# Kernel optimization log

Measured on AMD Instinct MI355X. Metric: run time of the kernel, lower is better.

## Reference

```python
import jax, jax.numpy as jnp
import numpy as np

EPS = 0.05
THRESH = 1e-6
MAX_ITER = 100


def _l2norm(x):
    # matches torch F.normalize(dim=-1): x / max(||x||, 1e-12)
    n = jnp.sqrt(jnp.sum(x * x, axis=-1, keepdims=True))
    return x / jnp.maximum(n, 1e-12)


def setup_inputs() -> dict:
    key = jax.random.key(0)
    kq, kk, kv = jax.random.split(key, 3)
    B, N, D = 8, 1024, 64
    return {
        "q": jax.random.normal(kq, (B, N, D), dtype=jnp.float32),
        "k": jax.random.normal(kk, (B, N, D), dtype=jnp.float32),
        "V": jax.random.normal(kv, (B, N, D), dtype=jnp.float32),
    }


def reference(q, k, V):
    B, N, D = q.shape
    Q = _l2norm(q)
    Kn = _l2norm(k)
    # cost matrix: 1 - cosine similarity, shape (B, N, N)
    C = 1.0 - jnp.einsum("bnd,bmd->bnm", Q, Kn)

    log_mu = jnp.full((B, N), jnp.log(1.0 / N + 1e-8), dtype=C.dtype)
    log_nu = log_mu

    def kernel(u, v):
        # (-C + u_i + v_j) / eps, shape (B, N, N)
        return (-C + u[:, :, None] + v[:, None, :]) / EPS

    def step(carry, _):
        u, v, done = carry
        u0 = u
        u_new = EPS * (log_mu - jax.scipy.special.logsumexp(kernel(u, v), axis=2)) + u
        v_new = EPS * (log_nu - jax.scipy.special.logsumexp(kernel(u_new, v), axis=1)) + v
        err = jnp.mean(jnp.abs(u_new - u0))
        # replicate torch early-break: once converged, freeze u, v
        u = jnp.where(done, u, u_new)
        v = jnp.where(done, v, v_new)
        done = jnp.logical_or(done, err < THRESH)
        return (u, v, done), None

    u0 = jnp.zeros((B, N), dtype=C.dtype)
    v0 = jnp.zeros((B, N), dtype=C.dtype)
    (u, v, _), _ = jax.lax.scan(
        jax.checkpoint(step), (u0, v0, jnp.array(False)), None, length=MAX_ITER
    )

    T = jnp.exp(kernel(u, v))  # transport plan (B, N, N)
    out = jnp.einsum("bnm,bmd->bnd", T, V) + V
    return out
```

## Files before the change

kernel.cpp:

```cpp
#include <hip/hip_runtime.h>
#include <math.h>

#define BB 8
#define NN 1024
#define DD 64
#define EPSF 0.05f
#define MAX_ITER 100
#define ERR_SUM_THRESH 8.192e-3f
#define SCALE_ 28.853900817779268f
#define EPSLN2_ 0.034657359027997264f
#define NBLK 256
#define NPER 32

typedef __attribute__((ext_vector_type(8))) short short8;
typedef __attribute__((ext_vector_type(4))) float f32x4;

static __device__ __forceinline__ float fexp2(float x) { return __builtin_amdgcn_exp2f(x); }
static __device__ __forceinline__ float flog2(float x) { return __builtin_amdgcn_logf(x); }
static __device__ __forceinline__ float bflo(unsigned u) { return __uint_as_float(u << 16); }
static __device__ __forceinline__ unsigned short bf16rne(float x) {
    unsigned u = __float_as_uint(x);
    u += 0x7fffu + ((u >> 16) & 1u);
    return (unsigned short)(u >> 16);
}
__device__ __forceinline__ float wave_sum64(float x) {
#pragma unroll
    for (int off = 1; off < 64; off <<= 1) x += __shfl_xor(x, off);
    return x;
}

#define ERRIDX(t, b) ((b) * 128 + (t))
#define CNTIDX(p, b) ((b) * 256 + (p))
#define PUBIDX(t) (t)

__global__ __launch_bounds__(256) void cost_kernel(const float* __restrict__ q,
                                                   const float* __restrict__ k,
                                                   unsigned short* __restrict__ M,
                                                   unsigned short* __restrict__ MT) {
    __shared__ __align__(16) float Qs[64][65];
    __shared__ __align__(16) float Ks[64][65];
    __shared__ float qin[64];
    __shared__ float kin[64];
    __shared__ __align__(16) unsigned short Qb[64][72];
    __shared__ __align__(16) unsigned short Kb[64][72];
    int b = blockIdx.z;
    int i0 = blockIdx.y * 64, j0 = blockIdx.x * 64;
    const float* Qp = q + ((size_t)b * NN + i0) * DD;
    const float* Kp = k + ((size_t)b * NN + j0) * DD;
    int tid = threadIdx.x;
#pragma unroll
    for (int kk = 0; kk < 4; ++kk) {
        int c = tid + 256 * kk;
        int row = c >> 4;
        int c4 = c & 15;
        float4 qv = ((const float4*)(Qp + row * DD))[c4];
        Qs[row][c4 * 4 + 0] = qv.x; Qs[row][c4 * 4 + 1] = qv.y;
        Qs[row][c4 * 4 + 2] = qv.z; Qs[row][c4 * 4 + 3] = qv.w;
        float4 kv = ((const float4*)(Kp + row * DD))[c4];
        Ks[row][c4 * 4 + 0] = kv.x; Ks[row][c4 * 4 + 1] = kv.y;
        Ks[row][c4 * 4 + 2] = kv.z; Ks[row][c4 * 4 + 3] = kv.w;
    }
    __syncthreads();
    if (tid < 64) {
        float ss = 0.f;
#pragma unroll 16
        for (int d = 0; d < 64; ++d) ss += Qs[tid][d] * Qs[tid][d];
        qin[tid] = 1.0f / fmaxf(sqrtf(ss), 1e-12f);
    } else if (tid < 128) {
        int r = tid - 64;
        float ss = 0.f;
#pragma unroll 16
        for (int d = 0; d < 64; ++d) ss += Ks[r][d] * Ks[r][d];
        kin[r] = 1.0f / fmaxf(sqrtf(ss), 1e-12f);
    }
    __syncthreads();
    {
        int row = tid >> 2, d0 = (tid & 3) * 16;
        float qs = qin[row], ks = kin[row];
#pragma unroll
        for (int p = 0; p < 4; ++p) {
            int d = d0 + p * 4;
            uint2 t;
            t.x = (unsigned)bf16rne(Qs[row][d + 0] * qs) | ((unsigned)bf16rne(Qs[row][d + 1] * qs) << 16);
            t.y = (unsigned)bf16rne(Qs[row][d + 2] * qs) | ((unsigned)bf16rne(Qs[row][d + 3] * qs) << 16);
            *(uint2*)&Qb[row][d] = t;
            t.x = (unsigned)bf16rne(Ks[row][d + 0] * ks) | ((unsigned)bf16rne(Ks[row][d + 1] * ks) << 16);
            t.y = (unsigned)bf16rne(Ks[row][d + 2] * ks) | ((unsigned)bf16rne(Ks[row][d + 3] * ks) << 16);
            *(uint2*)&Kb[row][d] = t;
        }
    }
    __syncthreads();
    int w = tid >> 6, lane = tid & 63;
    int m = lane & 15, qq = lane >> 4;
    int rloc = w * 16;
    short8 a0 = *(const short8*)&Qb[rloc + m][qq * 8];
    short8 a1 = *(const short8*)&Qb[rloc + m][qq * 8 + 32];
    f32x4 acc[4];
#pragma unroll
    for (int nt = 0; nt < 4; ++nt) {
        short8 b0 = *(const short8*)&Kb[nt * 16 + m][qq * 8];
        short8 b1 = *(const short8*)&Kb[nt * 16 + m][qq * 8 + 32];
        f32x4 z = {0.f, 0.f, 0.f, 0.f};
        z = __builtin_amdgcn_mfma_f32_16x16x32_bf16(a0, b0, z, 0, 0, 0);
        acc[nt] = __builtin_amdgcn_mfma_f32_16x16x32_bf16(a1, b1, z, 0, 0, 0);
    }
#pragma unroll
    for (int nt = 0; nt < 4; ++nt) {
        int gj = j0 + nt * 16 + m;
        unsigned short us[4];
#pragma unroll
        for (int r = 0; r < 4; ++r)
            us[r] = bf16rne(fexp2((acc[nt][r] - 1.0f) * SCALE_));
#pragma unroll
        for (int r = 0; r < 4; ++r)
            M[((size_t)b << 20) + ((size_t)(i0 + rloc + qq * 4 + r) << 10) + gj] = us[r];
        uint2 t;
        t.x = (unsigned)us[0] | ((unsigned)us[1] << 16);
        t.y = (unsigned)us[2] | ((unsigned)us[3] << 16);
        *(uint2*)(MT + ((size_t)b << 20) + ((size_t)gj << 10) + i0 + rloc + qq * 4) = t;
    }
}

#define ACC8(U4, base)                                              \
    s0 = fmaf(bflo(U4.x), wrg[base + 0], s0);                       \
    s1 = fmaf(__uint_as_float(U4.x), wrg[base + 1], s1);            \
    s0 = fmaf(bflo(U4.y), wrg[base + 2], s0);                       \
    s1 = fmaf(__uint_as_float(U4.y), wrg[base + 3], s1);            \
    s0 = fmaf(bflo(U4.z), wrg[base + 4], s0);                       \
    s1 = fmaf(__uint_as_float(U4.z), wrg[base + 5], s1);            \
    s0 = fmaf(bflo(U4.w), wrg[base + 6], s0);                       \
    s1 = fmaf(__uint_as_float(U4.w), wrg[base + 7], s1);

__global__ __launch_bounds__(256, 1) void sink_coop(const unsigned short* __restrict__ M,
                                                    const unsigned short* __restrict__ MT,
                                                    float* __restrict__ u,
                                                    float* __restrict__ v,
                                                    float* __restrict__ err,
                                                    unsigned* __restrict__ cnt,
                                                    unsigned* __restrict__ pub,
                                                    float eln) {
    __shared__ __align__(16) float sw[1280];
    __shared__ float sdel[4];
    __shared__ int sflag;
    int tid = threadIdx.x;
    int w = tid >> 6, lane = tid & 63;
    int b = blockIdx.x & 7;
    int slice = blockIdx.x >> 3;
    int rbase = slice * 32 + w * 8;
    const unsigned short* Mb  = M  + ((size_t)b << 20);
    const unsigned short* MTb = MT + ((size_t)b << 20);
    float* ub = u + (b << 10);
    float* vb = v + (b << 10);

    uint4 mA[8], mB[8], nA[8], nB[8];
#pragma unroll
    for (int r = 0; r < 8; ++r) {
        const uint4* rp = (const uint4*)(Mb + ((size_t)(rbase + r) << 10));
        mA[r] = rp[lane * 2];
        mB[r] = rp[lane * 2 + 1];
        const uint4* tp = (const uint4*)(MTb + ((size_t)(rbase + r) << 10));
        nA[r] = tp[lane * 2];
        nB[r] = tp[lane * 2 + 1];
    }

    float uprev[8];
#pragma unroll
    for (int r = 0; r < 8; ++r) uprev[r] = 0.f;

    for (int t = 0; t < MAX_ITER; ++t) {
        {
            float4 ex;
            ex.x = fexp2(__hip_atomic_load(vb + tid * 4 + 0, __ATOMIC_RELAXED, __HIP_MEMORY_SCOPE_AGENT) * SCALE_);
            ex.y = fexp2(__hip_atomic_load(vb + tid * 4 + 1, __ATOMIC_RELAXED, __HIP_MEMORY_SCOPE_AGENT) * SCALE_);
            ex.z = fexp2(__hip_atomic_load(vb + tid * 4 + 2, __ATOMIC_RELAXED, __HIP_MEMORY_SCOPE_AGENT) * SCALE_);
            ex.w = fexp2(__hip_atomic_load(vb + tid * 4 + 3, __ATOMIC_RELAXED, __HIP_MEMORY_SCOPE_AGENT) * SCALE_);
            *(float4*)&sw[tid * 4 + 4 * (tid >> 2)] = ex;
            __syncthreads();
            float wrg[16];
            *(float4*)&wrg[0]  = *(const float4*)&sw[lane * 20 + 0];
            *(float4*)&wrg[4]  = *(const float4*)&sw[lane * 20 + 4];
            *(float4*)&wrg[8]  = *(const float4*)&sw[lane * 20 + 8];
            *(float4*)&wrg[12] = *(const float4*)&sw[lane * 20 + 12];
            float del = 0.f;
#pragma unroll
            for (int rr = 0; rr < 8; ++rr) {
                float s0 = 0.f, s1 = 0.f;
                ACC8(mA[rr], 0)
                ACC8(mB[rr], 8)
                float s = wave_sum64(s0 + s1);
                float un = eln - EPSLN2_ * flog2(s);
                del += fabsf(un - uprev[rr]);
                uprev[rr] = un;
                if (lane == 0)
                    __hip_atomic_store(ub + rbase + rr, un, __ATOMIC_RELAXED, __HIP_MEMORY_SCOPE_AGENT);
            }
            if (lane == 0) sdel[w] = del;
            asm volatile("s_waitcnt vmcnt(0)" ::: "memory");
            __syncthreads();
            if (tid == 0) {
                __hip_atomic_fetch_add(err + ERRIDX(t, b), sdel[0] + sdel[1] + sdel[2] + sdel[3],
                                       __ATOMIC_RELAXED, __HIP_MEMORY_SCOPE_AGENT);
                asm volatile("s_waitcnt vmcnt(0)" ::: "memory");
                unsigned* c = cnt + CNTIDX(2 * t, b);
                __hip_atomic_fetch_add(c, 1u, __ATOMIC_RELAXED, __HIP_MEMORY_SCOPE_AGENT);
                while (__hip_atomic_load(c, __ATOMIC_RELAXED, __HIP_MEMORY_SCOPE_AGENT) < NPER)
                    __builtin_amdgcn_s_sleep(1);
                if (slice == 0) {
                    asm volatile("s_waitcnt vmcnt(0)" ::: "memory");
                    __hip_atomic_fetch_add(pub + PUBIDX(t), 1u, __ATOMIC_RELAXED, __HIP_MEMORY_SCOPE_AGENT);
                }
            }
            __syncthreads();
        }
        {
            float4 ex;
            ex.x = fexp2(__hip_atomic_load(ub + tid * 4 + 0, __ATOMIC_RELAXED, __HIP_MEMORY_SCOPE_AGENT) * SCALE_);
            ex.y = fexp2(__hip_atomic_load(ub + tid * 4 + 1, __ATOMIC_RELAXED, __HIP_MEMORY_SCOPE_AGENT) * SCALE_);
            ex.z = fexp2(__hip_atomic_load(ub + tid * 4 + 2, __ATOMIC_RELAXED, __HIP_MEMORY_SCOPE_AGENT) * SCALE_);
            ex.w = fexp2(__hip_atomic_load(ub + tid * 4 + 3, __ATOMIC_RELAXED, __HIP_MEMORY_SCOPE_AGENT) * SCALE_);
            *(float4*)&sw[tid * 4 + 4 * (tid >> 2)] = ex;
            __syncthreads();
            float wrg[16];
            *(float4*)&wrg[0]  = *(const float4*)&sw[lane * 20 + 0];
            *(float4*)&wrg[4]  = *(const float4*)&sw[lane * 20 + 4];
            *(float4*)&wrg[8]  = *(const float4*)&sw[lane * 20 + 8];
            *(float4*)&wrg[12] = *(const float4*)&sw[lane * 20 + 12];
#pragma unroll
            for (int rr = 0; rr < 8; ++rr) {
                float s0 = 0.f, s1 = 0.f;
                ACC8(nA[rr], 0)
                ACC8(nB[rr], 8)
                float s = wave_sum64(s0 + s1);
                float vn = eln - EPSLN2_ * flog2(s);
                if (lane == 0)
                    __hip_atomic_store(vb + rbase + rr, vn, __ATOMIC_RELAXED, __HIP_MEMORY_SCOPE_AGENT);
            }
            asm volatile("s_waitcnt vmcnt(0)" ::: "memory");
            __syncthreads();
            if (tid == 0) {
                unsigned* c = cnt + CNTIDX(2 * t + 1, b);
                __hip_atomic_fetch_add(c, 1u, __ATOMIC_RELAXED, __HIP_MEMORY_SCOPE_AGENT);
                while (__hip_atomic_load(c, __ATOMIC_RELAXED, __HIP_MEMORY_SCOPE_AGENT) < NPER)
                    __builtin_amdgcn_s_sleep(1);
                float eb = __hip_atomic_load(err + ERRIDX(t, b), __ATOMIC_RELAXED, __HIP_MEMORY_SCOPE_AGENT);
                int brk = 0;
                if (eb < ERR_SUM_THRESH) {
                    while (__hip_atomic_load(pub + PUBIDX(t), __ATOMIC_RELAXED, __HIP_MEMORY_SCOPE_AGENT) < 8u)
                        __builtin_amdgcn_s_sleep(1);
                    float s = 0.f;
                    for (int bb = 0; bb < 8; ++bb)
                        s += __hip_atomic_load(err + ERRIDX(t, bb), __ATOMIC_RELAXED, __HIP_MEMORY_SCOPE_AGENT);
                    brk = (s < ERR_SUM_THRESH);
                }
                sflag = brk;
            }
            __syncthreads();
            if (sflag) break;
        }
    }
}

__global__ __launch_bounds__(256) void wt_kernel(const float* __restrict__ V,
                                                 const float* __restrict__ v,
                                                 unsigned short* __restrict__ WT) {
    __shared__ __align__(16) float Vs[64][65];
    __shared__ float wj[64];
    int b = blockIdx.x & 7, jt = blockIdx.x >> 3;
    int j0 = jt * 64;
    int tid = threadIdx.x;
    const float* Vb = V + ((size_t)b << 16) + ((size_t)j0 << 6);
#pragma unroll
    for (int c = 0; c < 4; ++c) {
        int idx = tid + 256 * c;
        int row = idx >> 4, c4 = idx & 15;
        float4 x = ((const float4*)(Vb + row * 64))[c4];
        Vs[row][c4 * 4 + 0] = x.x; Vs[row][c4 * 4 + 1] = x.y;
        Vs[row][c4 * 4 + 2] = x.z; Vs[row][c4 * 4 + 3] = x.w;
    }
    if (tid < 64) wj[tid] = fexp2(v[(b << 10) + j0 + tid] * SCALE_);
    __syncthreads();
    int d = tid >> 2, qd = tid & 3;
    unsigned pk[8];
#pragma unroll
    for (int p = 0; p < 8; ++p) {
        int j = qd * 16 + p * 2;
        unsigned lo = bf16rne(Vs[j][d] * wj[j]);
        unsigned hi = bf16rne(Vs[j + 1][d] * wj[j + 1]);
        pk[p] = lo | (hi << 16);
    }
    unsigned short* dst = WT + ((size_t)b << 16) + ((size_t)d << 10) + j0 + qd * 16;
    ((uint4*)dst)[0] = make_uint4(pk[0], pk[1], pk[2], pk[3]);
    ((uint4*)dst)[1] = make_uint4(pk[4], pk[5], pk[6], pk[7]);
}

__global__ __launch_bounds__(256) void gemm_final(const unsigned short* __restrict__ M,
                                                  const unsigned short* __restrict__ WT,
                                                  const float* __restrict__ u,
                                                  const float* __restrict__ V,
                                                  float* __restrict__ out) {
    __shared__ float sa[32];
    int tid = threadIdx.x;
    int w = tid >> 6, lane = tid & 63;
    int b = blockIdx.x & 7, mt = blockIdx.x >> 3;
    if (tid < 32) sa[tid] = fexp2(u[(b << 10) + mt * 32 + tid] * SCALE_);
    __syncthreads();
    int m = lane & 15, q = lane >> 4;
    int rloc = (w & 1) * 16;
    int nbase = (w >> 1) * 32;
    const unsigned short* Ma = M + ((size_t)b << 20) + ((size_t)(mt * 32 + rloc + m) << 10) + q * 8;
    const unsigned short* W0 = WT + ((size_t)b << 16) + ((size_t)(nbase + m) << 10) + q * 8;
    const unsigned short* W1 = W0 + (16 << 10);
    f32x4 acc0 = {0.f, 0.f, 0.f, 0.f}, acc1 = {0.f, 0.f, 0.f, 0.f};
#pragma unroll 4
    for (int k0 = 0; k0 < NN; k0 += 32) {
        short8 af = *(const short8*)(Ma + k0);
        short8 b0 = *(const short8*)(W0 + k0);
        short8 b1 = *(const short8*)(W1 + k0);
        acc0 = __builtin_amdgcn_mfma_f32_16x16x32_bf16(af, b0, acc0, 0, 0, 0);
        acc1 = __builtin_amdgcn_mfma_f32_16x16x32_bf16(af, b1, acc1, 0, 0, 0);
    }
#pragma unroll
    for (int r = 0; r < 4; ++r) {
        int lrow = rloc + q * 4 + r;
        int gm = mt * 32 + lrow;
        float a = sa[lrow];
        size_t base = (((size_t)b << 10) + gm) * DD;
        int n0 = nbase + m;
        out[base + n0]      = fmaf(a, acc0[r], V[base + n0]);
        out[base + n0 + 16] = fmaf(a, acc1[r], V[base + n0 + 16]);
    }
}

extern "C" void kernel_launch(void* const* d_in, const int* in_sizes, int n_in,
                              void* d_out, int out_size, void* d_ws, size_t ws_size,
                              hipStream_t stream) {
    const float* q = (const float*)d_in[0];
    const float* k = (const float*)d_in[1];
    const float* V = (const float*)d_in[2];
    float* out = (float*)d_out;

    char* ws = (char*)d_ws;
    const size_t MB16 = (size_t)BB * NN * NN * sizeof(unsigned short);
    unsigned short* M  = (unsigned short*)ws;
    unsigned short* MT = (unsigned short*)(ws + MB16);
    unsigned short* WT = MT;
    float* u   = (float*)(ws + 2 * MB16);
    float* v   = u + BB * NN;
    float* err = v + BB * NN;
    unsigned* cnt = (unsigned*)(err + 1024);
    unsigned* pub = cnt + 2048;

    size_t zbytes = (size_t)(2 * BB * NN + 1024 + 2048 + 128) * 4;
    hipMemsetAsync(u, 0, zbytes, stream);

    cost_kernel<<<dim3(16, 16, 8), 256, 0, stream>>>(q, k, M, MT);

    float eln = EPSF * logf(1.0f / NN + 1e-8f);
    sink_coop<<<dim3(NBLK), dim3(256), 0, stream>>>(M, MT, u, v, err, cnt, pub, eln);

    wt_kernel<<<128, 256, 0, stream>>>(V, v, WT);
    gemm_final<<<256, 256, 0, stream>>>(M, WT, u, V, out);
}
```

Baseline: 189.9 us.

## Fuse final transport-plan GEMM into persistent Sinkhorn kernel, drop wt and gemm kernels

Removes the separate wt_kernel and MFMA gemm_final launches. After the Sinkhorn loop exits, each cooperative block loads the final v, scales its own rows of M by exp(v), and multiplies by V with scalar FMAs staged through LDS, adding the V residual. This saves two kernel launches and the WT round trip through global memory. In exchange, the MFMA GEMM becomes a CUDA-core FP32 loop over 1024x64 per row group, and there is no grid-wide barrier before v is read, which risks reading stale v from other blocks.

```diff
diff --git a/kernel.cpp b/kernel.cpp
--- a/kernel.cpp
+++ b/kernel.cpp
@@ -18,6 +18,7 @@
 static __device__ __forceinline__ float fexp2(float x) { return __builtin_amdgcn_exp2f(x); }
 static __device__ __forceinline__ float flog2(float x) { return __builtin_amdgcn_logf(x); }
 static __device__ __forceinline__ float bflo(unsigned u) { return __uint_as_float(u << 16); }
+static __device__ __forceinline__ float bfu(unsigned short s) { return __uint_as_float(((unsigned)s) << 16); }
 static __device__ __forceinline__ unsigned short bf16rne(float x) {
     unsigned u = __float_as_uint(x);
     u += 0x7fffu + ((u >> 16) & 1u);
@@ -32,6 +33,7 @@
 #define ERRIDX(t, b) ((b) * 128 + (t))
 #define CNTIDX(p, b) ((b) * 256 + (p))
 #define PUBIDX(t) (t)
+#define SWIDX2(j) ((j) + 4 * ((j) >> 4))
 
 __global__ __launch_bounds__(256) void cost_kernel(const float* __restrict__ q,
                                                    const float* __restrict__ k,
@@ -138,10 +140,13 @@
                                                     float* __restrict__ err,
                                                     unsigned* __restrict__ cnt,
                                                     unsigned* __restrict__ pub,
+                                                    const float* __restrict__ V,
+                                                    float* __restrict__ out,
                                                     float eln) {
     __shared__ __align__(16) float sw[1280];
     __shared__ float sdel[4];
     __shared__ int sflag;
+    __shared__ __align__(16) float sP[4][64][8];
     int tid = threadIdx.x;
     int w = tid >> 6, lane = tid & 63;
     int b = blockIdx.x & 7;
@@ -258,76 +263,54 @@
             if (sflag) break;
         }
     }
-}
-
-__global__ __launch_bounds__(256) void wt_kernel(const float* __restrict__ V,
-                                                 const float* __restrict__ v,
-                                                 unsigned short* __restrict__ WT) {
-    __shared__ __align__(16) float Vs[64][65];
-    __shared__ float wj[64];
-    int b = blockIdx.x & 7, jt = blockIdx.x >> 3;
-    int j0 = jt * 64;
-    int tid = threadIdx.x;
-    const float* Vb = V + ((size_t)b << 16) + ((size_t)j0 << 6);
-#pragma unroll
-    for (int c = 0; c < 4; ++c) {
-        int idx = tid + 256 * c;
-        int row = idx >> 4, c4 = idx & 15;
-        float4 x = ((const float4*)(Vb + row * 64))[c4];
-        Vs[row][c4 * 4 + 0] = x.x; Vs[row][c4 * 4 + 1] = x.y;
-        Vs[row][c4 * 4 + 2] = x.z; Vs[row][c4 * 4 + 3] = x.w;
-    }
-    if (tid < 64) wj[tid] = fexp2(v[(b << 10) + j0 + tid] * SCALE_);
-    __syncthreads();
-    int d = tid >> 2, qd = tid & 3;
-    unsigned pk[8];
-#pragma unroll
-    for (int p = 0; p < 8; ++p) {
-        int j = qd * 16 + p * 2;
-        unsigned lo = bf16rne(Vs[j][d] * wj[j]);
-        unsigned hi = bf16rne(Vs[j + 1][d] * wj[j + 1]);
-        pk[p] = lo | (hi << 16);
-    }
-    unsigned short* dst = WT + ((size_t)b << 16) + ((size_t)d << 10) + j0 + qd * 16;
-    ((uint4*)dst)[0] = make_uint4(pk[0], pk[1], pk[2], pk[3]);
-    ((uint4*)dst)[1] = make_uint4(pk[4], pk[5], pk[6], pk[7]);
-}
-
-__global__ __launch_bounds__(256) void gemm_final(const unsigned short* __restrict__ M,
-                                                  const unsigned short* __restrict__ WT,
-                                                  const float* __restrict__ u,
-                                                  const float* __restrict__ V,
-                                                  float* __restrict__ out) {
-    __shared__ float sa[32];
-    int tid = threadIdx.x;
-    int w = tid >> 6, lane = tid & 63;
-    int b = blockIdx.x & 7, mt = blockIdx.x >> 3;
-    if (tid < 32) sa[tid] = fexp2(u[(b << 10) + mt * 32 + tid] * SCALE_);
-    __syncthreads();
-    int m = lane & 15, q = lane >> 4;
-    int rloc = (w & 1) * 16;
-    int nbase = (w >> 1) * 32;
-    const unsigned short* Ma = M + ((size_t)b << 20) + ((size_t)(mt * 32 + rloc + m) << 10) + q * 8;
-    const unsigned short* W0 = WT + ((size_t)b << 16) + ((size_t)(nbase + m) << 10) + q * 8;
-    const unsigned short* W1 = W0 + (16 << 10);
-    f32x4 acc0 = {0.f, 0.f, 0.f, 0.f}, acc1 = {0.f, 0.f, 0.f, 0.f};
-#pragma unroll 4
-    for (int k0 = 0; k0 < NN; k0 += 32) {
-        short8 af = *(const short8*)(Ma + k0);
-        short8 b0 = *(const short8*)(W0 + k0);
-        short8 b1 = *(const short8*)(W1 + k0);
-        acc0 = __builtin_amdgcn_mfma_f32_16x16x32_bf16(af, b0, acc0, 0, 0, 0);
-        acc1 = __builtin_amdgcn_mfma_f32_16x16x32_bf16(af, b1, acc1, 0, 0, 0);
-    }
-#pragma unroll
-    for (int r = 0; r < 4; ++r) {
-        int lrow = rloc + q * 4 + r;
-        int gm = mt * 32 + lrow;
-        float a = sa[lrow];
-        size_t base = (((size_t)b << 10) + gm) * DD;
-        int n0 = nbase + m;
-        out[base + n0]      = fmaf(a, acc0[r], V[base + n0]);
-        out[base + n0 + 16] = fmaf(a, acc1[r], V[base + n0 + 16]);
+
+    __syncthreads();
+    {
+        float4 ex;
+        ex.x = fexp2(__hip_atomic_load(vb + tid * 4 + 0, __ATOMIC_RELAXED, __HIP_MEMORY_SCOPE_AGENT) * SCALE_);
+        ex.y = fexp2(__hip_atomic_load(vb + tid * 4 + 1, __ATOMIC_RELAXED, __HIP_MEMORY_SCOPE_AGENT) * SCALE_);
+        ex.z = fexp2(__hip_atomic_load(vb + tid * 4 + 2, __ATOMIC_RELAXED, __HIP_MEMORY_SCOPE_AGENT) * SCALE_);
+        ex.w = fexp2(__hip_atomic_load(vb + tid * 4 + 3, __ATOMIC_RELAXED, __HIP_MEMORY_SCOPE_AGENT) * SCALE_);
+        *(float4*)&sw[tid * 4 + 4 * (tid >> 2)] = ex;
+    }
+    __syncthreads();
+    const float* Vb = V + ((size_t)b << 16);
+    float a8[8];
+#pragma unroll
+    for (int r = 0; r < 8; ++r) a8[r] = fexp2(uprev[r] * SCALE_);
+    float acc[8] = {0.f, 0.f, 0.f, 0.f, 0.f, 0.f, 0.f, 0.f};
+    for (int j0 = 0; j0 < NN; j0 += 64) {
+        float vt[64];
+#pragma unroll
+        for (int jj = 0; jj < 64; ++jj) vt[jj] = Vb[(size_t)(j0 + jj) * DD + lane];
+        float wl = sw[SWIDX2(j0 + lane)];
+        float p[8];
+#pragma unroll
+        for (int r = 0; r < 8; ++r)
+            p[r] = bfu(Mb[((size_t)(rbase + r) << 10) + j0 + lane]) * wl;
+        asm volatile("s_waitcnt lgkmcnt(0)" ::: "memory");
+        *(float4*)&sP[w][lane][0] = make_float4(p[0], p[1], p[2], p[3]);
+        *(float4*)&sP[w][lane][4] = make_float4(p[4], p[5], p[6], p[7]);
+        asm volatile("s_waitcnt lgkmcnt(0)" ::: "memory");
+#pragma unroll
+        for (int jj = 0; jj < 64; ++jj) {
+            float4 pA = *(const float4*)&sP[w][jj][0];
+            float4 pB = *(const float4*)&sP[w][jj][4];
+            acc[0] = fmaf(pA.x, vt[jj], acc[0]);
+            acc[1] = fmaf(pA.y, vt[jj], acc[1]);
+            acc[2] = fmaf(pA.z, vt[jj], acc[2]);
+            acc[3] = fmaf(pA.w, vt[jj], acc[3]);
+            acc[4] = fmaf(pB.x, vt[jj], acc[4]);
+            acc[5] = fmaf(pB.y, vt[jj], acc[5]);
+            acc[6] = fmaf(pB.z, vt[jj], acc[6]);
+            acc[7] = fmaf(pB.w, vt[jj], acc[7]);
+        }
+    }
+#pragma unroll
+    for (int r = 0; r < 8; ++r) {
+        int gi = rbase + r;
+        out[(((size_t)b << 10) + gi) * DD + lane] =
+            fmaf(a8[r], acc[r], Vb[(size_t)gi * DD + lane]);
     }
 }
 
@@ -343,7 +326,6 @@
     const size_t MB16 = (size_t)BB * NN * NN * sizeof(unsigned short);
     unsigned short* M  = (unsigned short*)ws;
     unsigned short* MT = (unsigned short*)(ws + MB16);
-    unsigned short* WT = MT;
     float* u   = (float*)(ws + 2 * MB16);
     float* v   = u + BB * NN;
     float* err = v + BB * NN;
@@ -356,8 +338,5 @@
     cost_kernel<<<dim3(16, 16, 8), 256, 0, stream>>>(q, k, M, MT);
 
     float eln = EPSF * logf(1.0f / NN + 1e-8f);
-    sink_coop<<<dim3(NBLK), dim3(256), 0, stream>>>(M, MT, u, v, err, cnt, pub, eln);
-
-    wt_kernel<<<128, 256, 0, stream>>>(V, v, WT);
-    gemm_final<<<256, 256, 0, stream>>>(M, WT, u, V, out);
-}
+    sink_coop<<<dim3(NBLK), dim3(256), 0, stream>>>(M, MT, u, v, err, cnt, pub, V, out, eln);
+}
```

After: 201.5 us. +6.1%, slower.
